# Performance work log

Hardware: AMD Instinct MI355X
Metric: run time of the kernel (lower is better)

The kernel has to match this reference:

```python
import jax, jax.numpy as jnp
import numpy as np

H = 256                      # latent_channels = LSTM hidden
OC = [32, 64, 64, 128]       # out_channels per mesh level
V = [5023, 1256, 314, 79, 20]  # vertex counts per level (fine -> coarse)
L = 9                        # spiral length
T = 64                       # audio frames (batch for decoder)


def setup_inputs() -> dict:
    key = jax.random.key(0)
    ks = iter(jax.random.split(key, 80))
    f32 = jnp.float32

    def nrm(shape, fan_in):
        return jax.random.normal(next(ks), shape, f32) * (1.0 / np.sqrt(fan_in))

    inp = {}
    inp['audio'] = jax.random.normal(next(ks), (T, 768), f32)
    inp['actor'] = jax.random.normal(next(ks), (V[0], 3), f32)

    # 5-layer bidirectional LSTM; layer 0 input 768, layers 1-4 input 2H
    inp['lstm_Wih0'] = nrm((2, 4 * H, 768), 768)
    inp['lstm_Whh0'] = nrm((2, 4 * H, H), H)
    inp['lstm_b0'] = jnp.zeros((2, 4 * H), f32)
    inp['lstm_Wih'] = nrm((4, 2, 4 * H, 2 * H), 2 * H)
    inp['lstm_Whh'] = nrm((4, 2, 4 * H, H), H)
    inp['lstm_b'] = jnp.zeros((4, 2, 4 * H), f32)

    # decoder entry fc: 2*latent -> num_vert * oc[-1]
    inp['fc_W'] = nrm((V[4] * OC[3], 2 * H), 2 * H)
    inp['fc_b'] = jnp.zeros((V[4] * OC[3],), f32)

    # SpiralConv weights (torch Linear layout: [out, in*L])
    inp['conv3_W'] = nrm((128, 128 * L), 128 * L); inp['conv3_b'] = jnp.zeros((128,), f32)
    inp['conv2_W'] = nrm((64, 128 * L), 128 * L);  inp['conv2_b'] = jnp.zeros((64,), f32)
    inp['conv1_W'] = nrm((64, 64 * L), 64 * L);    inp['conv1_b'] = jnp.zeros((64,), f32)
    inp['conv0_W'] = nrm((32, 64 * L), 64 * L);    inp['conv0_b'] = jnp.zeros((32,), f32)
    inp['head_W'] = nrm((3, 32 * L), 32 * L);      inp['head_b'] = jnp.zeros((3,), f32)

    # spiral indices per level: [V_j, L] with values in [0, V_j)
    for j in range(4):
        inp[f'idx{j}'] = jax.random.randint(next(ks), (V[j], L), 0, V[j], jnp.int32)

    # up_transform[j] sparse [V_j, V_{j+1}], ~3 nnz per row (COO)
    for j in range(4):
        nnz = 3 * V[j]
        inp[f'rows{j}'] = jnp.repeat(jnp.arange(V[j], dtype=jnp.int32), 3)
        inp[f'cols{j}'] = jax.random.randint(next(ks), (nnz,), 0, V[j + 1], jnp.int32)
        inp[f'vals{j}'] = jax.random.uniform(next(ks), (nnz,), f32) / 3.0
    return inp


def _lstm_dir(x, Wih, Whh, b, reverse):
    # x: [T, Din]; torch gate order i, f, g, o
    def step(carry, xt):
        h, c = carry
        g = Wih @ xt + Whh @ h + b            # [4H]
        i, f, gg, o = jnp.split(g, 4)
        c = jax.nn.sigmoid(f) * c + jax.nn.sigmoid(i) * jnp.tanh(gg)
        h = jax.nn.sigmoid(o) * jnp.tanh(c)
        return (h, c), h
    init = (jnp.zeros((H,), x.dtype), jnp.zeros((H,), x.dtype))
    _, hs = jax.lax.scan(step, init, x, reverse=reverse)
    return hs  # [T, H], aligned with input order


def _bilstm(x, Wih, Whh, b):
    hf = _lstm_dir(x, Wih[0], Whh[0], b[0], False)
    hb = _lstm_dir(x, Wih[1], Whh[1], b[1], True)
    return jnp.concatenate([hf, hb], axis=-1)  # [T, 2H]


def _pool(x, rows, cols, vals, n_out):
    # sparse up-transform: out[t, r] = sum_nnz vals * x[t, cols]
    g = x[:, cols, :] * vals[None, :, None]                       # [T, nnz, C]
    return jax.ops.segment_sum(g.swapaxes(0, 1), rows, num_segments=n_out).swapaxes(0, 1)


def _spiral(x, idx, W, b):
    # gather fixed spiral neighborhoods then dense linear
    g = x[:, idx, :].reshape(x.shape[0], idx.shape[0], -1)        # [T, V, L*C]
    return g @ W.T + b


def reference(audio, actor, lstm_Wih0, lstm_Whh0, lstm_b0, lstm_Wih, lstm_Whh, lstm_b,
              fc_W, fc_b, conv3_W, conv3_b, conv2_W, conv2_b, conv1_W, conv1_b,
              conv0_W, conv0_b, head_W, head_b,
              vals3, vals2, vals1, vals0,
              idx0, idx1, idx2, idx3,
              rows3, cols3, rows2, cols2, rows1, cols1, rows0, cols0):
    # audio embedding: 5-layer bidirectional LSTM (batch = 1)
    z = _bilstm(audio, lstm_Wih0, lstm_Whh0, lstm_b0)
    for l in range(4):
        z = _bilstm(z, lstm_Wih[l], lstm_Whh[l], lstm_b[l])       # [T, 2H]

    # decode
    x = (z @ fc_W.T + fc_b).reshape(z.shape[0], V[4], OC[3])      # [T, 20, 128]
    x = jax.nn.elu(_spiral(_pool(x, rows3, cols3, vals3, V[3]), idx3, conv3_W, conv3_b))
    x = jax.nn.elu(_spiral(_pool(x, rows2, cols2, vals2, V[2]), idx2, conv2_W, conv2_b))
    x = jax.nn.elu(_spiral(_pool(x, rows1, cols1, vals1, V[1]), idx1, conv1_W, conv1_b))
    x = jax.nn.elu(_spiral(_pool(x, rows0, cols0, vals0, V[0]), idx0, conv0_W, conv0_b))
    x = _spiral(x, idx0, head_W, head_b)                          # [T, 5023, 3]
    return x + actor[None]
```

## Files before the change

kernel.cpp:

```cpp
#include <hip/hip_runtime.h>
#include <hip/hip_bf16.h>

typedef __attribute__((ext_vector_type(8))) __bf16 bf16x8;
typedef __attribute__((ext_vector_type(4))) float  f32x4;
typedef __attribute__((ext_vector_type(4))) int    i32x4;

#define SCOPE_AGENT __HIP_MEMORY_SCOPE_AGENT

static __device__ __forceinline__ f32x4 mfma16(bf16x8 a, bf16x8 b, f32x4 c) {
    return __builtin_amdgcn_mfma_f32_16x16x32_bf16(a, b, c, 0, 0, 0);
}
static __device__ __forceinline__ i32x4 mfma_i8(i32x4 a, i32x4 b, i32x4 c) {
    return __builtin_amdgcn_mfma_i32_16x16x64_i8(a, b, c, 0, 0, 0);
}
static __device__ __forceinline__ float sigm(float x)  { return 1.0f / (1.0f + __expf(-x)); }
static __device__ __forceinline__ float tanh_(float x) { return 1.0f - 2.0f / (__expf(2.0f * x) + 1.0f); }

static __device__ __forceinline__ bf16x8 cvt8(const float* __restrict__ p) {
    const float4* q = (const float4*)p;
    float4 a = q[0], b = q[1];
    bf16x8 r;
    r[0] = (__bf16)a.x; r[1] = (__bf16)a.y; r[2] = (__bf16)a.z; r[3] = (__bf16)a.w;
    r[4] = (__bf16)b.x; r[5] = (__bf16)b.y; r[6] = (__bf16)b.z; r[7] = (__bf16)b.w;
    return r;
}
static __device__ __forceinline__ void signal_add(unsigned int* p) {
    __hip_atomic_fetch_add(p, 1u, __ATOMIC_RELEASE, SCOPE_AGENT);
}
template <int SLP>
static __device__ __forceinline__ void wait_eq(unsigned int* p, unsigned int v) {
    while (__hip_atomic_load(p, __ATOMIC_RELAXED, SCOPE_AGENT) != v)
        __builtin_amdgcn_s_sleep(SLP);
    (void)__hip_atomic_load(p, __ATOMIC_ACQUIRE, SCOPE_AGENT);
}
union g4u { unsigned long long q; __bf16 h[4]; };

#define ZBUF_OFF   1024
#define GX_OFF     132096
#define CONVW_OFF  66560
#define ARENA_A    621248
#define ARENA_B    21195456
#define WHHQ_BOFF  11534336
#define SWP_BOFF   14155776
#define O_WIH0  0
#define O_WIHL  1572864

__global__ __launch_bounds__(256) void precvt_lstm(
    const float* __restrict__ Wih0, const float* __restrict__ WihL,
    const float* __restrict__ Whh0, const float* __restrict__ WhhL,
    __bf16* __restrict__ out, signed char* __restrict__ WhhQ,
    float* __restrict__ swp)
{
    const int bid = blockIdx.x;
    if (bid < 5632) {
        int f = (bid * 256 + threadIdx.x) * 4;
        const float* src; int off;
        if (f < 1572864) { src = Wih0; off = f; }
        else             { src = WihL; off = f - 1572864; }
        float4 v = *(const float4*)(src + off);
        g4u u;
        u.h[0] = (__bf16)v.x; u.h[1] = (__bf16)v.y; u.h[2] = (__bf16)v.z; u.h[3] = (__bf16)v.w;
        *(unsigned long long*)(out + f) = u.q;
        return;
    }
    const int g  = (bid - 5632) * 4 + (threadIdx.x >> 6);
    const int dl = g >> 10;
    const int r  = g & 1023;
    const int lane = threadIdx.x & 63;
    const float* src = (dl < 2 ? Whh0 + (size_t)dl * 262144
                               : WhhL + (size_t)(dl - 2) * 262144) + (size_t)r * 256;
    float4 v = *(const float4*)(src + lane * 4);
    float am = fmaxf(fmaxf(fabsf(v.x), fabsf(v.y)), fmaxf(fabsf(v.z), fabsf(v.w)));
    #pragma unroll
    for (int m = 1; m < 64; m <<= 1) am = fmaxf(am, __shfl_xor(am, m));
    const float inv = am > 0.f ? 127.f / am : 0.f;
    int q0 = __float2int_rn(v.x * inv), q1 = __float2int_rn(v.y * inv);
    int q2 = __float2int_rn(v.z * inv), q3 = __float2int_rn(v.w * inv);
    unsigned pk = (q0 & 255) | ((q1 & 255) << 8) | ((q2 & 255) << 16) | ((q3 & 255) << 24);
    const int gate = r >> 8, cell = r & 255;
    const int m  = cell * 4 + gate;
    const int ln = m & 15, mt = m >> 4;
    const int k  = lane * 4;
    const int kc = k >> 6, quad = (k >> 4) & 3, j = k & 15;
    size_t addr = ((((size_t)dl * 64 + mt) * 4 + kc) * 64 + (quad * 16 + ln)) * 16 + j;
    *(unsigned*)(WhhQ + addr) = pk;
    if (lane == 0) swp[(size_t)dl * 1024 + cell * 4 + gate] = am / 127.f;
}

__global__ __launch_bounds__(256) void precvt_dec(
    const float* __restrict__ fcW, const float* __restrict__ c3W,
    const float* __restrict__ c2W, const float* __restrict__ c1W,
    const float* __restrict__ c0W, const float* __restrict__ hW,
    __bf16* __restrict__ fcWb, __bf16* __restrict__ convWb)
{
    int f = (blockIdx.x * 256 + threadIdx.x) * 4;
    if (f >= 1588064) return;
    const float* src; int off; __bf16* dst; int doff;
    if (f < 1310720) { src = fcW; off = f; dst = fcWb; doff = f; }
    else {
        int g = f - 1310720; dst = convWb; doff = g;
        if (g < 147456)      { src = c3W; off = g; }
        else if (g < 221184) { src = c2W; off = g - 147456; }
        else if (g < 258048) { src = c1W; off = g - 221184; }
        else if (g < 276480) { src = c0W; off = g - 258048; }
        else                 { src = hW;  off = g - 276480; }
    }
    float4 v = *(const float4*)(src + off);
    g4u u;
    u.h[0] = (__bf16)v.x; u.h[1] = (__bf16)v.y; u.h[2] = (__bf16)v.z; u.h[3] = (__bf16)v.w;
    *(unsigned long long*)(dst + doff) = u.q;
}

__global__ __launch_bounds__(512) __attribute__((amdgpu_waves_per_eu(2, 2)))
void lstm_fused(
    const float* __restrict__ audio,
    const __bf16* __restrict__ WihB,
    const signed char* __restrict__ WhhQ,
    const float* __restrict__ swp,
    const float* __restrict__ b0, const float* __restrict__ bL,
    unsigned short* __restrict__ Gx_g,
    unsigned int* __restrict__ flags,
    unsigned short* __restrict__ zbuf)
{
    const int bid = blockIdx.x;
    const int tid = threadIdx.x;
    const int wave = tid >> 6, lane = tid & 63, ln = lane & 15, quad = lane >> 4;

    __shared__ __align__(16) signed char    hq[2][256];
    __shared__ __align__(16) signed char    zq[16384];
    __shared__ __align__(16) unsigned short gx_l[65536];

    if (bid < 16) {
        const int dir = bid >> 3, sub = bid & 7;
        const int gmt = sub * 8 + wave;
        for (int l = 0; l < 5; ++l) {
            if (l > 0) {
                if (tid == 0) wait_eq<4>(&flags[32 + (l - 1)], 2u);
                __syncthreads();
            }
            const int Din = l ? 512 : 768;
            const __bf16* Wih_l = l ? (WihB + O_WIHL + (size_t)((l - 1) * 2 + dir) * 524288)
                                    : (WihB + (size_t)dir * 786432);
            const float* b_l = l ? (bL + (size_t)((l - 1) * 2 + dir) * 1024)
                                 : (b0 + (size_t)dir * 1024);
            const __bf16* zp = (const __bf16*)(zbuf + (size_t)((l - 1) & 1) * 32768);

            f32x4 acc[4];
            #pragma unroll
            for (int nt = 0; nt < 4; ++nt) acc[nt] = (f32x4){0.f, 0.f, 0.f, 0.f};
            const int m_a = gmt * 16 + ln;
            const int r_a = (m_a & 3) * 256 + (m_a >> 2);
            const int Kc = Din >> 5;
            for (int kc = 0; kc < Kc; ++kc) {
                const int k0 = kc * 32 + quad * 8;
                bf16x8 afr = *(const bf16x8*)(Wih_l + (size_t)r_a * Din + k0);
                #pragma unroll
                for (int nt = 0; nt < 4; ++nt) {
                    const int t = nt * 16 + ln;
                    bf16x8 bfr = l ? *(const bf16x8*)(zp + (size_t)t * 512 + k0)
                                   : cvt8(audio + (size_t)t * 768 + k0);
                    acc[nt] = mfma16(afr, bfr, acc[nt]);
                }
            }
            float bv[4];
            #pragma unroll
            for (int reg = 0; reg < 4; ++reg) {
                const int m_row = gmt * 16 + quad * 4 + reg;
                bv[reg] = b_l[(m_row & 3) * 256 + (m_row >> 2)];
            }
            #pragma unroll
            for (int nt = 0; nt < 4; ++nt) {
                #pragma unroll
                for (int reg = 0; reg < 4; ++reg) {
                    const int m_row = gmt * 16 + quad * 4 + reg;
                    const int t = nt * 16 + ln;
                    __bf16 v = (__bf16)(acc[nt][reg] + bv[reg]);
                    Gx_g[(size_t)dir * 65536 + t * 1024 + m_row] =
                        __builtin_bit_cast(unsigned short, v);
                }
            }
            __syncthreads();
            if (tid == 0) { __threadfence(); signal_add(&flags[l * 2 + dir]); }
        }
    } else {
        const int dir = bid - 16;
        const unsigned short* Gx_d = Gx_g + (size_t)dir * 65536;
        const bool owner = (ln < 8);
        const int cell = wave * 32 + ln * 4 + quad;
        const int gcell = owner ? cell : 0;

        for (int l = 0; l < 5; ++l) {
            const int dl = l * 2 + dir;
            i32x4 wf[8][4];
            const i32x4* wb = (const i32x4*)(WhhQ + (size_t)dl * 262144);
            #pragma unroll
            for (int i = 0; i < 8; ++i)
                #pragma unroll
                for (int kc = 0; kc < 4; ++kc)
                    wf[i][kc] = wb[(size_t)(((wave * 8 + i) * 4 + kc)) * 64 + lane];
            float sc0 = 0.f, sc1 = 0.f, sc2 = 0.f, sc3 = 0.f;
            if (owner) {
                float4 s4 = *(const float4*)(swp + (size_t)dl * 1024 + cell * 4);
                const float f = 1.f / 127.f;
                sc0 = s4.x * f; sc1 = s4.y * f; sc2 = s4.z * f; sc3 = s4.w * f;
            }
            if (tid == 0) wait_eq<1>(&flags[l * 2 + dir], 8u);
            __syncthreads();
            {
                const float4* src = (const float4*)Gx_d;
                float4* dst = (float4*)gx_l;
                #pragma unroll
                for (int i = 0; i < 16; ++i) dst[i * 512 + tid] = src[i * 512 + tid];
            }
            if (tid < 64) ((unsigned int*)hq[0])[tid] = 0;
            float cst = 0.f;
            __syncthreads();

            for (int s = 0; s < 64; ++s) {
                const int t = dir ? (63 - s) : s;
                const int cur = s & 1, nxt = cur ^ 1;
                g4u gx;
                gx.q = *(const unsigned long long*)&gx_l[t * 1024 + gcell * 4];
                i32x4 acc[8];
                #pragma unroll
                for (int i = 0; i < 8; ++i) acc[i] = (i32x4){0, 0, 0, 0};
                #pragma unroll
                for (int kc = 0; kc < 4; ++kc) {
                    i32x4 b = *(const i32x4*)&hq[cur][kc * 64 + quad * 16];
                    #pragma unroll
                    for (int i = 0; i < 8; ++i) acc[i] = mfma_i8(wf[i][kc], b, acc[i]);
                }
                i32x4 a = acc[0];
                #pragma unroll
                for (int j = 1; j < 8; ++j) if (ln == j) a = acc[j];
                if (owner) {
                    float gi = (float)a[0] * sc0 + (float)gx.h[0];
                    float gf = (float)a[1] * sc1 + (float)gx.h[1];
                    float gg = (float)a[2] * sc2 + (float)gx.h[2];
                    float go = (float)a[3] * sc3 + (float)gx.h[3];
                    cst = sigm(gf) * cst + sigm(gi) * tanh_(gg);
                    float h = sigm(go) * tanh_(cst);
                    int q = __float2int_rn(h * 127.f);
                    hq[nxt][cell] = (signed char)q;
                    zq[t * 256 + cell] = (signed char)q;
                }
                __syncthreads();
            }
            unsigned short* zl = zbuf + (size_t)(l & 1) * 32768;
            #pragma unroll
            for (int i = 0; i < 8; ++i) {
                const int idx = i * 512 + tid;
                const int tt = idx >> 6, cb = (idx & 63) * 4;
                unsigned u = ((const unsigned*)zq)[idx];
                g4u o;
                #pragma unroll
                for (int j = 0; j < 4; ++j) {
                    int b = (int)(signed char)(u >> (8 * j));
                    o.h[j] = (__bf16)((float)b * (1.f / 127.f));
                }
                *(unsigned long long*)(zl + (size_t)tt * 512 + dir * 256 + cb) = o.q;
            }
            __syncthreads();
            if (tid == 0) { __threadfence(); signal_add(&flags[32 + l]); }
        }
    }
}

__global__ __launch_bounds__(256) void fc_kernel(
    const __bf16* __restrict__ zb, const __bf16* __restrict__ W,
    const float* __restrict__ bb, __bf16* __restrict__ out)
{
    const int tid = threadIdx.x;
    const int wave = tid >> 6, lane = tid & 63, ln = lane & 15, quad = lane >> 4;
    const int nbase = blockIdx.x * 64;
    f32x4 acc[4];
    #pragma unroll
    for (int nt = 0; nt < 4; nt++) acc[nt] = (f32x4){0.f, 0.f, 0.f, 0.f};
    #pragma unroll 2
    for (int kc = 0; kc < 16; kc++) {
        const int k0 = kc * 32 + quad * 8;
        bf16x8 a = *(const bf16x8*)(zb + (size_t)(wave * 16 + ln) * 512 + k0);
        #pragma unroll
        for (int nt = 0; nt < 4; nt++) {
            bf16x8 b = *(const bf16x8*)(W + (size_t)(nbase + nt * 16 + ln) * 512 + k0);
            acc[nt] = mfma16(a, b, acc[nt]);
        }
    }
    #pragma unroll
    for (int nt = 0; nt < 4; nt++) {
        const int n = nbase + nt * 16 + ln;
        const float bv = bb[n];
        #pragma unroll
        for (int reg = 0; reg < 4; reg++) {
            const int t = wave * 16 + quad * 4 + reg;
            out[(size_t)((n >> 7) * 64 + t) * 128 + (n & 127)] = (__bf16)(acc[nt][reg] + bv);
        }
    }
}

template <int C>
__global__ __launch_bounds__(256) void pool_kernel(
    const __bf16* __restrict__ in, __bf16* __restrict__ out,
    const int* __restrict__ cols, const float* __restrict__ vals, int V)
{
    const int P = 64 * C / 8;
    const int gid = blockIdx.x * 256 + threadIdx.x;
    if (gid >= V * P) return;
    const int r = gid / P;
    const int rem = gid - r * P;
    float acc[8] = {0.f, 0.f, 0.f, 0.f, 0.f, 0.f, 0.f, 0.f};
    #pragma unroll
    for (int s = 0; s < 3; s++) {
        const int col = cols[3 * r + s];
        const float vv = vals[3 * r + s];
        bf16x8 x = *(const bf16x8*)(in + (size_t)col * 64 * C + rem * 8);
        #pragma unroll
        for (int e = 0; e < 8; e++) acc[e] += vv * (float)x[e];
    }
    bf16x8 ov;
    #pragma unroll
    for (int e = 0; e < 8; e++) ov[e] = (__bf16)acc[e];
    *(bf16x8*)(out + (size_t)r * 64 * C + rem * 8) = ov;
}

template <int CIN, int COUT>
__global__ __launch_bounds__(256) void conv_kernel(
    const __bf16* __restrict__ in, __bf16* __restrict__ out,
    const int* __restrict__ idx, const __bf16* __restrict__ W,
    const float* __restrict__ bias)
{
    constexpr int K = 9 * CIN;
    constexpr int NT = COUT / 16;
    constexpr int NKC = K / 32;
    const int v = blockIdx.x;
    const int tid = threadIdx.x;
    const int wave = tid >> 6, lane = tid & 63, ln = lane & 15, quad = lane >> 4;
    __shared__ int sIdx[9];
    if (tid < 9) sIdx[tid] = idx[v * 9 + tid];
    __syncthreads();
    f32x4 acc[NT];
    #pragma unroll
    for (int nt = 0; nt < NT; nt++) acc[nt] = (f32x4){0.f, 0.f, 0.f, 0.f};
    const int tt = wave * 16 + ln;
    for (int kc = 0; kc < NKC; kc++) {
        const int k0 = kc * 32;
        const int l = k0 / CIN;
        const int c = (k0 & (CIN - 1)) + quad * 8;
        const int row = sIdx[l];
        bf16x8 a = *(const bf16x8*)(in + ((size_t)row * 64 + tt) * CIN + c);
        #pragma unroll
        for (int nt = 0; nt < NT; nt++) {
            bf16x8 b = *(const bf16x8*)(W + (size_t)(nt * 16 + ln) * K + k0 + quad * 8);
            acc[nt] = mfma16(a, b, acc[nt]);
        }
    }
    #pragma unroll
    for (int nt = 0; nt < NT; nt++) {
        const int n = nt * 16 + ln;
        const float bv = bias[n];
        #pragma unroll
        for (int reg = 0; reg < 4; reg++) {
            const int t = wave * 16 + quad * 4 + reg;
            float val = acc[nt][reg] + bv;
            val = val > 0.f ? val : (__expf(val) - 1.f);
            out[((size_t)v * 64 + t) * COUT + n] = (__bf16)val;
        }
    }
}

__global__ __launch_bounds__(256) void head_kernel(
    const __bf16* __restrict__ in, float* __restrict__ out,
    const int* __restrict__ idx, const __bf16* __restrict__ W,
    const float* __restrict__ bias, const float* __restrict__ actor)
{
    const int v = blockIdx.x;
    const int tid = threadIdx.x;
    const int wave = tid >> 6, lane = tid & 63, ln = lane & 15, quad = lane >> 4;
    __shared__ int sIdx[9];
    if (tid < 9) sIdx[tid] = idx[v * 9 + tid];
    __syncthreads();
    f32x4 acc = (f32x4){0.f, 0.f, 0.f, 0.f};
    const int tt = wave * 16 + ln;
    const int rown = ln < 3 ? ln : 0;
    #pragma unroll
    for (int kc = 0; kc < 9; kc++) {
        const int row = sIdx[kc];
        bf16x8 a = *(const bf16x8*)(in + ((size_t)row * 64 + tt) * 32 + quad * 8);
        bf16x8 b = *(const bf16x8*)(W + (size_t)rown * 288 + kc * 32 + quad * 8);
        acc = mfma16(a, b, acc);
    }
    if (ln < 3) {
        const float bv = bias[ln];
        const float av = actor[v * 3 + ln];
        #pragma unroll
        for (int reg = 0; reg < 4; reg++) {
            const int t = wave * 16 + quad * 4 + reg;
            out[((size_t)t * 5023 + v) * 3 + ln] = acc[reg] + bv + av;
        }
    }
}

extern "C" void kernel_launch(void* const* d_in, const int* in_sizes, int n_in,
                              void* d_out, int out_size, void* d_ws, size_t ws_size,
                              hipStream_t stream) {
    const float* audio = (const float*)d_in[0];
    const float* actor = (const float*)d_in[1];
    const float* Wih0  = (const float*)d_in[2];
    const float* Whh0  = (const float*)d_in[3];
    const float* b0    = (const float*)d_in[4];
    const float* WihL  = (const float*)d_in[5];
    const float* WhhL  = (const float*)d_in[6];
    const float* bLs   = (const float*)d_in[7];
    const float* fcW   = (const float*)d_in[8];
    const float* fcb   = (const float*)d_in[9];
    const float* c3W = (const float*)d_in[10]; const float* c3b = (const float*)d_in[11];
    const float* c2W = (const float*)d_in[12]; const float* c2b = (const float*)d_in[13];
    const float* c1W = (const float*)d_in[14]; const float* c1b = (const float*)d_in[15];
    const float* c0W = (const float*)d_in[16]; const float* c0b = (const float*)d_in[17];
    const float* hW  = (const float*)d_in[18]; const float* hb  = (const float*)d_in[19];
    const int* idx0 = (const int*)d_in[20];
    const int* idx1 = (const int*)d_in[21];
    const int* idx2 = (const int*)d_in[22];
    const int* idx3 = (const int*)d_in[23];
    const int* cols0 = (const int*)d_in[25]; const float* vals0 = (const float*)d_in[26];
    const int* cols1 = (const int*)d_in[28]; const float* vals1 = (const float*)d_in[29];
    const int* cols2 = (const int*)d_in[31]; const float* vals2 = (const float*)d_in[32];
    const int* cols3 = (const int*)d_in[34]; const float* vals3 = (const float*)d_in[35];

    char* ws = (char*)d_ws;
    unsigned int*   flags = (unsigned int*)ws;
    unsigned short* zbuf  = (unsigned short*)(ws + ZBUF_OFF);
    unsigned short* GxG   = (unsigned short*)(ws + GX_OFF);
    __bf16*         convWb = (__bf16*)(ws + CONVW_OFF);
    char* arenaA = ws + ARENA_A;
    char* arenaB = ws + ARENA_B;

    __bf16*      lw   = (__bf16*)arenaB;
    signed char* whhq = (signed char*)(arenaB + WHHQ_BOFF);
    float*       swp  = (float*)(arenaB + SWP_BOFF);
    __bf16*      fcWb = (__bf16*)(arenaB + 2097152);

    __bf16* x4b = (__bf16*)arenaA;
    __bf16* p3  = (__bf16*)arenaB;
    __bf16* c3o = (__bf16*)arenaA;
    __bf16* p2  = (__bf16*)arenaB;
    __bf16* c2o = (__bf16*)arenaA;
    __bf16* p1  = (__bf16*)arenaB;
    __bf16* c1o = (__bf16*)arenaA;
    __bf16* p0  = (__bf16*)arenaB;
    __bf16* c0o = (__bf16*)arenaA;

    (void)hipMemsetAsync(ws, 0, 1024, stream);

    precvt_lstm<<<8192, 256, 0, stream>>>(Wih0, WihL, Whh0, WhhL, lw, whhq, swp);
    lstm_fused<<<18, 512, 0, stream>>>(audio, lw, whhq, swp, b0, bLs,
                                       GxG, flags, zbuf);
    precvt_dec<<<1552, 256, 0, stream>>>(fcW, c3W, c2W, c1W, c0W, hW, fcWb, convWb);

    fc_kernel<<<40, 256, 0, stream>>>((const __bf16*)zbuf, fcWb, fcb, x4b);

    { int n = 79 * 64 * 128 / 8;
      pool_kernel<128><<<(n + 255) / 256, 256, 0, stream>>>(x4b, p3, cols3, vals3, 79);
      conv_kernel<128, 128><<<79, 256, 0, stream>>>(p3, c3o, idx3, convWb + 0, c3b); }
    { int n = 314 * 64 * 128 / 8;
      pool_kernel<128><<<(n + 255) / 256, 256, 0, stream>>>(c3o, p2, cols2, vals2, 314);
      conv_kernel<128, 64><<<314, 256, 0, stream>>>(p2, c2o, idx2, convWb + 147456, c2b); }
    { int n = 1256 * 64 * 64 / 8;
      pool_kernel<64><<<(n + 255) / 256, 256, 0, stream>>>(c2o, p1, cols1, vals1, 1256);
      conv_kernel<64, 64><<<1256, 256, 0, stream>>>(p1, c1o, idx1, convWb + 221184, c1b); }
    { int n = 5023 * 64 * 64 / 8;
      pool_kernel<64><<<(n + 255) / 256, 256, 0, stream>>>(c1o, p0, cols0, vals0, 5023);
      conv_kernel<64, 32><<<5023, 256, 0, stream>>>(p0, c0o, idx0, convWb + 258048, c0b); }

    head_kernel<<<5023, 256, 0, stream>>>(c0o, (float*)d_out, idx0, convWb + 276480, hb, actor);
}
```

Measured before the change: 958.4 us.

## Drop Wih bf16 pre-conversion and prefetch layer weights before inter-layer wait

The separate pass that converts the input-to-hidden LSTM weights to bf16 is removed. The fused LSTM kernel now reads fp32 weights directly and converts them in registers. For layers 1-4, each wave loads its Wih fragments into registers before waiting on the previous layer's completion flag, so that weight traffic overlaps the recurrent wait. The recurrent int8 MFMA loop also seeds its accumulators from the first MFMA instead of zero-initialising them. The costs are extra register pressure from holding 16 bf16x8 fragments and double the bytes read per weight load.

```diff
diff --git a/kernel.cpp b/kernel.cpp
--- a/kernel.cpp
+++ b/kernel.cpp
@@ -42,28 +42,12 @@
 #define ARENA_B    21195456
 #define WHHQ_BOFF  11534336
 #define SWP_BOFF   14155776
-#define O_WIH0  0
-#define O_WIHL  1572864
-
-__global__ __launch_bounds__(256) void precvt_lstm(
-    const float* __restrict__ Wih0, const float* __restrict__ WihL,
+
+__global__ __launch_bounds__(256) void precvt_whh(
     const float* __restrict__ Whh0, const float* __restrict__ WhhL,
-    __bf16* __restrict__ out, signed char* __restrict__ WhhQ,
-    float* __restrict__ swp)
-{
-    const int bid = blockIdx.x;
-    if (bid < 5632) {
-        int f = (bid * 256 + threadIdx.x) * 4;
-        const float* src; int off;
-        if (f < 1572864) { src = Wih0; off = f; }
-        else             { src = WihL; off = f - 1572864; }
-        float4 v = *(const float4*)(src + off);
-        g4u u;
-        u.h[0] = (__bf16)v.x; u.h[1] = (__bf16)v.y; u.h[2] = (__bf16)v.z; u.h[3] = (__bf16)v.w;
-        *(unsigned long long*)(out + f) = u.q;
-        return;
-    }
-    const int g  = (bid - 5632) * 4 + (threadIdx.x >> 6);
+    signed char* __restrict__ WhhQ, float* __restrict__ swp)
+{
+    const int g  = blockIdx.x * 4 + (threadIdx.x >> 6);
     const int dl = g >> 10;
     const int r  = g & 1023;
     const int lane = threadIdx.x & 63;
@@ -114,7 +98,8 @@
 __global__ __launch_bounds__(512) __attribute__((amdgpu_waves_per_eu(2, 2)))
 void lstm_fused(
     const float* __restrict__ audio,
-    const __bf16* __restrict__ WihB,
+    const float* __restrict__ Wih0,
+    const float* __restrict__ WihL,
     const signed char* __restrict__ WhhQ,
     const float* __restrict__ swp,
     const float* __restrict__ b0, const float* __restrict__ bL,
@@ -133,32 +118,22 @@
     if (bid < 16) {
         const int dir = bid >> 3, sub = bid & 7;
         const int gmt = sub * 8 + wave;
-        for (int l = 0; l < 5; ++l) {
-            if (l > 0) {
-                if (tid == 0) wait_eq<4>(&flags[32 + (l - 1)], 2u);
-                __syncthreads();
-            }
-            const int Din = l ? 512 : 768;
-            const __bf16* Wih_l = l ? (WihB + O_WIHL + (size_t)((l - 1) * 2 + dir) * 524288)
-                                    : (WihB + (size_t)dir * 786432);
-            const float* b_l = l ? (bL + (size_t)((l - 1) * 2 + dir) * 1024)
-                                 : (b0 + (size_t)dir * 1024);
-            const __bf16* zp = (const __bf16*)(zbuf + (size_t)((l - 1) & 1) * 32768);
-
+        const int m_a = gmt * 16 + ln;
+        const int r_a = (m_a & 3) * 256 + (m_a >> 2);
+
+        {
+            const float* Wih_l = Wih0 + (size_t)dir * 786432;
+            const float* b_l   = b0 + (size_t)dir * 1024;
             f32x4 acc[4];
             #pragma unroll
             for (int nt = 0; nt < 4; ++nt) acc[nt] = (f32x4){0.f, 0.f, 0.f, 0.f};
-            const int m_a = gmt * 16 + ln;
-            const int r_a = (m_a & 3) * 256 + (m_a >> 2);
-            const int Kc = Din >> 5;
-            for (int kc = 0; kc < Kc; ++kc) {
+            for (int kc = 0; kc < 24; ++kc) {
                 const int k0 = kc * 32 + quad * 8;
-                bf16x8 afr = *(const bf16x8*)(Wih_l + (size_t)r_a * Din + k0);
+                bf16x8 afr = cvt8(Wih_l + (size_t)r_a * 768 + k0);
                 #pragma unroll
                 for (int nt = 0; nt < 4; ++nt) {
                     const int t = nt * 16 + ln;
-                    bf16x8 bfr = l ? *(const bf16x8*)(zp + (size_t)t * 512 + k0)
-                                   : cvt8(audio + (size_t)t * 768 + k0);
+                    bf16x8 bfr = cvt8(audio + (size_t)t * 768 + k0);
                     acc[nt] = mfma16(afr, bfr, acc[nt]);
                 }
             }
@@ -169,7 +144,7 @@
                 bv[reg] = b_l[(m_row & 3) * 256 + (m_row >> 2)];
             }
             #pragma unroll
-            for (int nt = 0; nt < 4; ++nt) {
+            for (int nt = 0; nt < 4; ++nt)
                 #pragma unroll
                 for (int reg = 0; reg < 4; ++reg) {
                     const int m_row = gmt * 16 + quad * 4 + reg;
@@ -178,7 +153,50 @@
                     Gx_g[(size_t)dir * 65536 + t * 1024 + m_row] =
                         __builtin_bit_cast(unsigned short, v);
                 }
-            }
+            __syncthreads();
+            if (tid == 0) { __threadfence(); signal_add(&flags[0 * 2 + dir]); }
+        }
+
+        for (int l = 1; l < 5; ++l) {
+            const float* Wih_l = WihL + (size_t)((l - 1) * 2 + dir) * 524288;
+            const float* b_l   = bL + (size_t)((l - 1) * 2 + dir) * 1024;
+            bf16x8 afr[16];
+            #pragma unroll
+            for (int kc = 0; kc < 16; ++kc)
+                afr[kc] = cvt8(Wih_l + (size_t)r_a * 512 + kc * 32 + quad * 8);
+            if (tid == 0) wait_eq<4>(&flags[32 + (l - 1)], 2u);
+            __syncthreads();
+            const __bf16* zp = (const __bf16*)(zbuf + (size_t)((l - 1) & 1) * 32768);
+
+            f32x4 acc[4];
+            #pragma unroll
+            for (int nt = 0; nt < 4; ++nt) acc[nt] = (f32x4){0.f, 0.f, 0.f, 0.f};
+            #pragma unroll 4
+            for (int kc = 0; kc < 16; ++kc) {
+                const int k0 = kc * 32 + quad * 8;
+                #pragma unroll
+                for (int nt = 0; nt < 4; ++nt) {
+                    const int t = nt * 16 + ln;
+                    bf16x8 bfr = *(const bf16x8*)(zp + (size_t)t * 512 + k0);
+                    acc[nt] = mfma16(afr[kc], bfr, acc[nt]);
+                }
+            }
+            float bv[4];
+            #pragma unroll
+            for (int reg = 0; reg < 4; ++reg) {
+                const int m_row = gmt * 16 + quad * 4 + reg;
+                bv[reg] = b_l[(m_row & 3) * 256 + (m_row >> 2)];
+            }
+            #pragma unroll
+            for (int nt = 0; nt < 4; ++nt)
+                #pragma unroll
+                for (int reg = 0; reg < 4; ++reg) {
+                    const int m_row = gmt * 16 + quad * 4 + reg;
+                    const int t = nt * 16 + ln;
+                    __bf16 v = (__bf16)(acc[nt][reg] + bv[reg]);
+                    Gx_g[(size_t)dir * 65536 + t * 1024 + m_row] =
+                        __builtin_bit_cast(unsigned short, v);
+                }
             __syncthreads();
             if (tid == 0) { __threadfence(); signal_add(&flags[l * 2 + dir]); }
         }
@@ -188,6 +206,7 @@
         const bool owner = (ln < 8);
         const int cell = wave * 32 + ln * 4 + quad;
         const int gcell = owner ? cell : 0;
+        const i32x4 czero = (i32x4){0, 0, 0, 0};
 
         for (int l = 0; l < 5; ++l) {
             const int dl = l * 2 + dir;
@@ -222,10 +241,13 @@
                 g4u gx;
                 gx.q = *(const unsigned long long*)&gx_l[t * 1024 + gcell * 4];
                 i32x4 acc[8];
-                #pragma unroll
-                for (int i = 0; i < 8; ++i) acc[i] = (i32x4){0, 0, 0, 0};
-                #pragma unroll
-                for (int kc = 0; kc < 4; ++kc) {
+                {
+                    i32x4 b0v = *(const i32x4*)&hq[cur][quad * 16];
+                    #pragma unroll
+                    for (int i = 0; i < 8; ++i) acc[i] = mfma_i8(wf[i][0], b0v, czero);
+                }
+                #pragma unroll
+                for (int kc = 1; kc < 4; ++kc) {
                     i32x4 b = *(const i32x4*)&hq[cur][kc * 64 + quad * 16];
                     #pragma unroll
                     for (int i = 0; i < 8; ++i) acc[i] = mfma_i8(wf[i][kc], b, acc[i]);
@@ -435,7 +457,6 @@
     char* arenaA = ws + ARENA_A;
     char* arenaB = ws + ARENA_B;
 
-    __bf16*      lw   = (__bf16*)arenaB;
     signed char* whhq = (signed char*)(arenaB + WHHQ_BOFF);
     float*       swp  = (float*)(arenaB + SWP_BOFF);
     __bf16*      fcWb = (__bf16*)(arenaB + 2097152);
@@ -452,8 +473,8 @@
 
     (void)hipMemsetAsync(ws, 0, 1024, stream);
 
-    precvt_lstm<<<8192, 256, 0, stream>>>(Wih0, WihL, Whh0, WhhL, lw, whhq, swp);
-    lstm_fused<<<18, 512, 0, stream>>>(audio, lw, whhq, swp, b0, bLs,
+    precvt_whh<<<2560, 256, 0, stream>>>(Whh0, WhhL, whhq, swp);
+    lstm_fused<<<18, 512, 0, stream>>>(audio, Wih0, WihL, whhq, swp, b0, bLs,
                                        GxG, flags, zbuf);
     precvt_dec<<<1552, 256, 0, stream>>>(fcW, c3W, c2W, c1W, c0W, hW, fcWb, convWb);
 
```

Result: no change. 949.9 us (-0.9%).
